# Kernel optimization log

Hardware: AMD Instinct MI355X
Metric: run time of the kernel (lower is better)

Reference implementation:

```python
import jax, jax.numpy as jnp
import numpy as np

R, N, B, S = 20, 4096, 16, 256          # relations, total nodes, graphs, nodes per graph
DIN, HID, H = 512, 128, 4               # in_dim, hidden_dim, num_heads
D = HID * H                              # flattened node-feature width (=512)
E = 16384                                # edges per relation
NEG_SLOPE = 0.2


def _gat(h, src, dst, W, al, ar, b):
    # DGL GATConv, eval mode (dropout off), identity residual (in == H*out), allow_zero_in_degree
    z = (h @ W).reshape(N, H, HID)                        # [N,H,Dh]
    el = (z * al).sum(-1)                                 # [N,H]
    er = (z * ar).sum(-1)                                 # [N,H]
    e = jax.nn.leaky_relu(el[src] + er[dst], NEG_SLOPE)   # [E,H]
    m = jax.ops.segment_max(e, dst, num_segments=N)       # per-dst max (edge softmax)
    ex = jnp.exp(e - m[dst])
    den = jax.ops.segment_sum(ex, dst, num_segments=N)
    alpha = ex / den[dst]                                 # [E,H]
    agg = jax.ops.segment_sum(alpha[..., None] * z[src], dst, num_segments=N)
    return agg + h.reshape(N, H, HID) + b, alpha


def _rgat_conv(h, src, dst, W, al, ar, b):
    # HeteroGraphConv with aggregate='mean' over R relations; scan keeps memory flat
    def body(acc, xs):
        s, d, Wr, alr, arr, br = xs
        out, alpha = _gat(h, s, d, Wr, alr, arr, br)
        return acc + out, alpha.mean(-1)                  # attention meaned over heads -> [E]
    acc, attn = jax.lax.scan(body, jnp.zeros((N, H, HID), h.dtype), (src, dst, W, al, ar, b))
    return acc / R, attn                                  # [N,H,Dh], [R,E]


def setup_inputs() -> dict:
    key = jax.random.key(0)
    ks = jax.random.split(key, 24)
    f32 = jnp.float32
    p = lambda k, shape: jax.random.normal(k, shape, f32) * 0.05
    z = lambda shape: jnp.zeros(shape, f32)
    return {
        'feat': jax.random.normal(ks[0], (N, DIN), f32),
        'hyp_emb': jax.random.normal(ks[1], (B, D), f32),
        'edge_src': jax.random.randint(ks[2], (R, E), 0, N),
        'edge_dst': jax.random.randint(ks[3], (R, E), 0, N),
        'W1': p(ks[4], (R, DIN, H * HID)), 'al1': p(ks[5], (R, H, HID)), 'ar1': p(ks[6], (R, H, HID)), 'b1': z((R, H, HID)),
        'W2': p(ks[7], (R, D, H * HID)), 'al2': p(ks[8], (R, H, HID)), 'ar2': p(ks[9], (R, H, HID)), 'b2': z((R, H, HID)),
        'Wq': p(ks[10], (D, D)), 'bq': z(D), 'Wk': p(ks[11], (D, D)), 'bk': z(D),
        'Wv': p(ks[12], (D, D)), 'bv': z(D), 'Wo': p(ks[13], (D, D)), 'bo': z(D),
        'Wn1': p(ks[14], (2 * D, HID)), 'bn1': z(HID), 'Wn2': p(ks[15], (HID, 2)), 'bn2': z(2),
    }


def reference(feat, hyp_emb, edge_src, edge_dst,
              W1, al1, ar1, b1, W2, al2, ar2, b2,
              Wq, bq, Wk, bk, Wv, bv, Wo, bo, Wn1, bn1, Wn2, bn2):
    # --- RGAT (rgat_generation) layer 1 + attention weights ---
    h1, attn = _rgat_conv(feat, edge_src, edge_dst, W1, al1, ar1, b1)
    h1 = jax.nn.elu(h1.reshape(N, D))
    # --- layer 2 ---
    h2, _ = _rgat_conv(h1, edge_src, edge_dst, W2, al2, ar2, b2)
    feats = h2.reshape(N, D)
    # --- node importance: scatter-add edge attention onto dst nodes, summed over etypes ---
    imp = jax.ops.segment_sum(attn.reshape(-1), edge_dst.reshape(-1), num_segments=N)
    feats_p = feats.reshape(B, S, D)                      # uniform graphs: split+pad == reshape
    weighted = feats_p * imp.reshape(B, S)[..., None]
    # --- MultiheadAttention(embed=D, heads=4): query = hyp_emb broadcast to all S positions ---
    Hm, Dm = 4, D // 4
    q = (hyp_emb @ Wq + bq).reshape(B, Hm, 1, Dm)         # identical query at every position
    k = (feats_p @ Wk + bk).reshape(B, S, Hm, Dm).transpose(0, 2, 1, 3)
    v = (feats_p @ Wv + bv).reshape(B, S, Hm, Dm).transpose(0, 2, 1, 3)
    scores = jnp.einsum('bhqd,bhkd->bhqk', q, k) / jnp.sqrt(jnp.float32(Dm))
    a = jax.nn.softmax(scores, axis=-1)                   # [B,Hm,1,S]
    ctx = jnp.einsum('bhqk,bhkd->bhqd', a, v).reshape(B, 1, D)
    attn_out = jnp.broadcast_to(ctx @ Wo + bo, (B, S, D))
    # --- node classifier on concat(weighted feats, attention output) ---
    combined = jnp.concatenate([weighted, attn_out], axis=-1).reshape(N, 2 * D)
    node_logits = jax.nn.relu(combined @ Wn1 + bn1) @ Wn2 + bn2
    return node_logits, attn
```

## Files before the change

kernel.cpp:

```cpp
#include <hip/hip_runtime.h>
#include <hip/hip_bf16.h>
#include <math.h>

#define NREL 20
#define NN   4096
#define NE   16384
#define DF   512
#define NHD  4
#define DHH  128
#define NB   16
#define NS   256

typedef __attribute__((ext_vector_type(8))) __bf16 bf16x8;
typedef __attribute__((ext_vector_type(4))) float f32x4;

__device__ inline float bf2f(unsigned short u) {
    union { float f; unsigned int i; } c; c.i = ((unsigned int)u) << 16; return c.f;
}
__device__ inline unsigned short f2bu(float f) {
    union { __hip_bfloat16 b; unsigned short u; } c; c.b = __float2bfloat16(f); return c.u;
}
__device__ inline void storeOut(float* p, float v) { *p = v; }
__device__ inline void storeOut(__hip_bfloat16* p, float v) { *p = __float2bfloat16(v); }

__device__ inline void load_lds16(const __hip_bfloat16* g, __hip_bfloat16* l) {
    __builtin_amdgcn_global_load_lds(
        (const __attribute__((address_space(1))) unsigned int*)(const void*)g,
        (__attribute__((address_space(3))) unsigned int*)(void*)l, 16, 0, 0);
}

__global__ void count_kernel(const int* __restrict__ dst, int* __restrict__ cnt) {
    int idx = blockIdx.x * 256 + threadIdx.x;
    int r = idx / NE;
    atomicAdd(&cnt[r * NN + dst[idx]], 1);
}

__global__ void sumcnt_kernel(const int* __restrict__ cnt, int* __restrict__ cntAll) {
    int n = blockIdx.x * 256 + threadIdx.x;
    int s = 0;
    #pragma unroll
    for (int r = 0; r < NREL; ++r) s += cnt[r * NN + n];
    cntAll[n] = s;
}

__global__ void scan_kernel(const int* __restrict__ cnt, int* __restrict__ rowptr,
                            int* __restrict__ woff) {
    int r = blockIdx.x;
    int t = threadIdx.x;
    __shared__ int sums[1024];
    int v[4]; int local = 0;
    #pragma unroll
    for (int j = 0; j < 4; ++j) { v[j] = cnt[r * NN + t * 4 + j]; local += v[j]; }
    sums[t] = local;
    __syncthreads();
    for (int off = 1; off < 1024; off <<= 1) {
        int x = (t >= off) ? sums[t - off] : 0;
        __syncthreads();
        sums[t] += x;
        __syncthreads();
    }
    int run = (t == 0) ? 0 : sums[t - 1];
    #pragma unroll
    for (int j = 0; j < 4; ++j) {
        rowptr[r * (NN + 1) + t * 4 + j] = run;
        woff[r * NN + t * 4 + j] = run;
        run += v[j];
    }
    if (t == 1023) rowptr[r * (NN + 1) + NN] = run;
}

__global__ void fill_kernel(const int* __restrict__ dst, const int* __restrict__ src,
                            int* __restrict__ woff, int* __restrict__ srcCSR,
                            int* __restrict__ eidCSR) {
    int idx = blockIdx.x * 256 + threadIdx.x;
    int r = idx / NE; int e = idx % NE;
    int pos = atomicAdd(&woff[r * NN + dst[idx]], 1);
    srcCSR[r * NE + pos] = src[idx];
    eidCSR[r * NE + pos] = e;
}

__global__ void cast_kernel(const float* __restrict__ in, unsigned short* __restrict__ out) {
    int i = blockIdx.x * 256 + threadIdx.x;
    float4 v = ((const float4*)in)[i];
    ushort4 o;
    o.x = f2bu(v.x); o.y = f2bu(v.y); o.z = f2bu(v.z); o.w = f2bu(v.w);
    ((ushort4*)out)[i] = o;
}

__global__ void biassum_kernel(const float* __restrict__ bmat, float* __restrict__ bsum) {
    int f = blockIdx.x * 256 + threadIdx.x;
    float s = 0.f;
    #pragma unroll
    for (int r = 0; r < NREL; ++r) s += bmat[r * DF + f];
    bsum[f] = s;
}

__global__ __launch_bounds__(256) void transw_kernel(
    const float* __restrict__ W, __hip_bfloat16* __restrict__ Wt, int K, int N)
{
    int r = blockIdx.z;
    __shared__ float t[32][33];
    int k0 = blockIdx.x * 32, n0 = blockIdx.y * 32;
    int tx = threadIdx.x % 32, ty = threadIdx.x / 32;
    #pragma unroll
    for (int kk = ty; kk < 32; kk += 8)
        t[kk][tx] = W[((size_t)r * K + k0 + kk) * N + n0 + tx];
    __syncthreads();
    #pragma unroll
    for (int nn = ty; nn < 32; nn += 8)
        Wt[((size_t)r * N + n0 + nn) * K + k0 + tx] = __float2bfloat16(t[tx][nn]);
}

template <typename OutT, bool RELU>
__global__ __launch_bounds__(256) void mfma_gemm(
    const __hip_bfloat16* __restrict__ A,
    const __hip_bfloat16* __restrict__ BtAll,
    const float* __restrict__ bias,
    OutT* __restrict__ Call, int M, int N, int K)
{
    int r = blockIdx.z;
    const __hip_bfloat16* Bt = BtAll + (size_t)r * N * K;
    OutT* C = Call + (size_t)r * M * N;
    const int rowBase = blockIdx.y * 128;
    const int colBase = blockIdx.x * 128;
    __shared__ __hip_bfloat16 As[128 * 32];
    __shared__ __hip_bfloat16 Bs[128 * 32];
    const int tid = threadIdx.x;
    const int w = tid >> 6, l = tid & 63;
    const int wr = w >> 1, wc = w & 1;
    const int m15 = l & 15, q = l >> 4;
    const int sRow = w * 16 + (l >> 2);
    const int sK = (l & 3) * 8;
    const __hip_bfloat16* Ag0 = A + (size_t)(rowBase + sRow) * K + sK;
    const __hip_bfloat16* Ag1 = Ag0 + (size_t)64 * K;
    const __hip_bfloat16* Bg0 = Bt + (size_t)(colBase + sRow) * K + sK;
    const __hip_bfloat16* Bg1 = Bg0 + (size_t)64 * K;
    __hip_bfloat16* Asl0 = As + sRow * 32 + sK;
    __hip_bfloat16* Asl1 = Asl0 + 2048;
    __hip_bfloat16* Bsl0 = Bs + sRow * 32 + sK;
    __hip_bfloat16* Bsl1 = Bsl0 + 2048;

    f32x4 acc[4][4];
    #pragma unroll
    for (int i = 0; i < 4; ++i)
        #pragma unroll
        for (int j = 0; j < 4; ++j) acc[i][j] = (f32x4){0.f, 0.f, 0.f, 0.f};

    for (int k0 = 0; k0 < K; k0 += 32) {
        load_lds16(Ag0 + k0, Asl0);
        load_lds16(Ag1 + k0, Asl1);
        load_lds16(Bg0 + k0, Bsl0);
        load_lds16(Bg1 + k0, Bsl1);
        __syncthreads();
        bf16x8 a[4], b[4];
        #pragma unroll
        for (int i = 0; i < 4; ++i)
            a[i] = *(const bf16x8*)&As[(wr * 64 + i * 16 + m15) * 32 + q * 8];
        #pragma unroll
        for (int j = 0; j < 4; ++j)
            b[j] = *(const bf16x8*)&Bs[(wc * 64 + j * 16 + m15) * 32 + q * 8];
        #pragma unroll
        for (int i = 0; i < 4; ++i)
            #pragma unroll
            for (int j = 0; j < 4; ++j)
                acc[i][j] = __builtin_amdgcn_mfma_f32_16x16x32_bf16(a[i], b[j], acc[i][j], 0, 0, 0);
        __syncthreads();
    }

    #pragma unroll
    for (int i = 0; i < 4; ++i) {
        #pragma unroll
        for (int j = 0; j < 4; ++j) {
            int col = colBase + wc * 64 + j * 16 + m15;
            float bv = bias ? bias[col] : 0.f;
            #pragma unroll
            for (int reg = 0; reg < 4; ++reg) {
                int row = rowBase + wr * 64 + i * 16 + q * 4 + reg;
                float v = acc[i][j][reg] + bv;
                if (RELU) v = fmaxf(v, 0.f);
                storeOut(&C[(size_t)row * N + col], v);
            }
        }
    }
}

template <typename OutT>
__global__ __launch_bounds__(256) void gemm_kernel(
    const float* __restrict__ A, const float* __restrict__ Bm,
    const float* __restrict__ bias, OutT* __restrict__ C,
    int M, int K, int Nn)
{
    int r = blockIdx.z;
    const float* B = Bm + (size_t)r * K * Nn;
    OutT* Cr = C + (size_t)r * M * Nn;
    int rowBase = blockIdx.y * 64;
    int colBase = blockIdx.x * 64;
    __shared__ float As[64][17];
    __shared__ float Bs[16][64];
    int tid = threadIdx.x;
    int tx = tid % 16, ty = tid / 16;
    float acc[4][4] = {};
    int aRow = tid / 4, aK4 = (tid % 4) * 4;
    int bK = tid / 16, bN4 = (tid % 16) * 4;
    for (int k0 = 0; k0 < K; k0 += 16) {
        int gRow = rowBase + aRow;
        float4 av = make_float4(0.f, 0.f, 0.f, 0.f);
        if (gRow < M) av = *(const float4*)(A + (size_t)gRow * K + k0 + aK4);
        As[aRow][aK4 + 0] = av.x; As[aRow][aK4 + 1] = av.y;
        As[aRow][aK4 + 2] = av.z; As[aRow][aK4 + 3] = av.w;
        float4 bv = *(const float4*)(B + (size_t)(k0 + bK) * Nn + colBase + bN4);
        *(float4*)&Bs[bK][bN4] = bv;
        __syncthreads();
        #pragma unroll
        for (int k = 0; k < 16; ++k) {
            float a[4], b[4];
            #pragma unroll
            for (int i = 0; i < 4; ++i) a[i] = As[ty * 4 + i][k];
            #pragma unroll
            for (int j = 0; j < 4; ++j) b[j] = Bs[k][tx * 4 + j];
            #pragma unroll
            for (int i = 0; i < 4; ++i)
                #pragma unroll
                for (int j = 0; j < 4; ++j) acc[i][j] += a[i] * b[j];
        }
        __syncthreads();
    }
    #pragma unroll
    for (int i = 0; i < 4; ++i) {
        int gRow = rowBase + ty * 4 + i;
        if (gRow >= M) continue;
        #pragma unroll
        for (int j = 0; j < 4; ++j) {
            int gCol = colBase + tx * 4 + j;
            float v = acc[i][j];
            if (bias) v += bias[gCol];
            storeOut(&Cr[(size_t)gRow * Nn + gCol], v);
        }
    }
}

__global__ __launch_bounds__(256) void eler_kernel(
    const __hip_bfloat16* __restrict__ Z, const float* __restrict__ al,
    const float* __restrict__ ar, float* __restrict__ el, float* __restrict__ er)
{
    int gw = (blockIdx.x * 256 + threadIdx.x) / 64;
    int lane = threadIdx.x & 63;
    int h = lane >> 4;
    int r = gw / NN, n = gw % NN;
    const __hip_bfloat16* zp = Z + ((size_t)(r * NN + n)) * DF + lane * 8;
    float4 raw = *(const float4*)zp;
    const unsigned short* u = (const unsigned short*)&raw;
    float pel = 0.f, per_ = 0.f;
    #pragma unroll
    for (int j = 0; j < 8; ++j) {
        int f = lane * 8 + j;
        float z = bf2f(u[j]);
        pel  += z * al[r * DF + f];
        per_ += z * ar[r * DF + f];
    }
    #pragma unroll
    for (int off = 1; off < 16; off <<= 1) {
        pel  += __shfl_xor(pel, off);
        per_ += __shfl_xor(per_, off);
    }
    if ((lane & 15) == 0) {
        el[((size_t)r * NN + n) * NHD + h] = pel;
        er[((size_t)r * NN + n) * NHD + h] = per_;
    }
}

__global__ __launch_bounds__(256) void alpha_kernel(
    const float* __restrict__ el, const float* __restrict__ er,
    const int* __restrict__ rowptr, const int* __restrict__ rowptr2,
    const int* __restrict__ cnt, const int* __restrict__ srcCSR,
    const int* __restrict__ eidCSR,
    float* __restrict__ alphaPk, int* __restrict__ srcPk,
    float* __restrict__ attn, float* __restrict__ imp)
{
    int t = blockIdx.x * 256 + threadIdx.x;
    int r = t / NN, n = t % NN;
    int start = rowptr[r * (NN + 1) + n];
    int d = rowptr[r * (NN + 1) + n + 1] - start;
    if (d == 0) return;
    float4 er4 = *(const float4*)&er[((size_t)r * NN + n) * NHD];
    float4 den = make_float4(0.f, 0.f, 0.f, 0.f);
    for (int j = 0; j < d; ++j) {
        int s = srcCSR[r * NE + start + j];
        float4 el4 = *(const float4*)&el[((size_t)r * NN + s) * NHD];
        float v0 = el4.x + er4.x; v0 = v0 > 0.f ? v0 : 0.2f * v0;
        float v1 = el4.y + er4.y; v1 = v1 > 0.f ? v1 : 0.2f * v1;
        float v2 = el4.z + er4.z; v2 = v2 > 0.f ? v2 : 0.2f * v2;
        float v3 = el4.w + er4.w; v3 = v3 > 0.f ? v3 : 0.2f * v3;
        den.x += __expf(v0); den.y += __expf(v1);
        den.z += __expf(v2); den.w += __expf(v3);
    }
    float4 inv = make_float4(1.f / den.x, 1.f / den.y, 1.f / den.z, 1.f / den.w);
    int pbase = rowptr2[n];
    for (int rp = 0; rp < r; ++rp) pbase += cnt[rp * NN + n];
    float impLoc = 0.f;
    for (int j = 0; j < d; ++j) {
        int s = srcCSR[r * NE + start + j];
        float4 el4 = *(const float4*)&el[((size_t)r * NN + s) * NHD];
        float v0 = el4.x + er4.x; v0 = v0 > 0.f ? v0 : 0.2f * v0;
        float v1 = el4.y + er4.y; v1 = v1 > 0.f ? v1 : 0.2f * v1;
        float v2 = el4.z + er4.z; v2 = v2 > 0.f ? v2 : 0.2f * v2;
        float v3 = el4.w + er4.w; v3 = v3 > 0.f ? v3 : 0.2f * v3;
        float4 a4 = make_float4(__expf(v0) * inv.x, __expf(v1) * inv.y,
                                __expf(v2) * inv.z, __expf(v3) * inv.w);
        *(float4*)&alphaPk[(size_t)(pbase + j) * 4] = a4;
        srcPk[pbase + j] = r * NN + s;
        if (attn) {
            float a = 0.25f * (a4.x + a4.y + a4.z + a4.w);
            attn[r * NE + eidCSR[r * NE + start + j]] = a;
            impLoc += a;
        }
    }
    if (attn) atomicAdd(&imp[n], impLoc);
}

__global__ __launch_bounds__(256) void aggc_kernel(
    const __hip_bfloat16* __restrict__ Z,
    const int* __restrict__ rowptr2, const int* __restrict__ srcPk,
    const float* __restrict__ alphaPk, const float* __restrict__ bsum,
    const float* __restrict__ hin, float* __restrict__ hout,
    __hip_bfloat16* __restrict__ hout_bf, int applyElu)
{
    int n = blockIdx.x;
    int w = threadIdx.x >> 6, lane = threadIdx.x & 63;
    int h = lane >> 4;
    int base = rowptr2[n];
    int deg = rowptr2[n + 1] - base;
    float acc[8] = {};
    int i = w;
    int nzrow = 0; float nalpha = 0.f;
    if (i < deg) {
        nzrow = srcPk[base + i];
        nalpha = alphaPk[(size_t)(base + i) * 4 + h];
    }
    while (i < deg) {
        int zrow = nzrow; float alpha = nalpha;
        int i2 = i + 4;
        if (i2 < deg) {
            nzrow = srcPk[base + i2];
            nalpha = alphaPk[(size_t)(base + i2) * 4 + h];
        }
        float4 raw = *(const float4*)&Z[(size_t)zrow * DF + lane * 8];
        const unsigned short* u = (const unsigned short*)&raw;
        #pragma unroll
        for (int j = 0; j < 8; ++j) acc[j] += alpha * bf2f(u[j]);
        i = i2;
    }
    __shared__ float red[4][DF];
    #pragma unroll
    for (int j = 0; j < 8; ++j) red[w][lane * 8 + j] = acc[j];
    __syncthreads();
    const float invR = 1.0f / NREL;
    int f = threadIdx.x;
    #pragma unroll
    for (int rep = 0; rep < 2; ++rep, f += 256) {
        float v = red[0][f] + red[1][f] + red[2][f] + red[3][f];
        v = (v + bsum[f]) * invR + hin[(size_t)n * DF + f];
        if (applyElu) v = v > 0.f ? v : expm1f(v);
        hout[(size_t)n * DF + f] = v;
        hout_bf[(size_t)n * DF + f] = __float2bfloat16(v);
    }
}

__global__ __launch_bounds__(256) void mha_scores(
    const float* __restrict__ q, const float* __restrict__ k,
    float* __restrict__ scores)
{
    int b = blockIdx.x;
    int w = threadIdx.x >> 6, lane = threadIdx.x & 63;
    int s = blockIdx.y * 4 + w;
    const float4* qp = (const float4*)&q[(size_t)b * DF + lane * 8];
    const float4* kp = (const float4*)&k[((size_t)(b * NS + s)) * DF + lane * 8];
    float4 q0 = qp[0], q1 = qp[1];
    float4 k0 = kp[0], k1 = kp[1];
    float p = q0.x * k0.x + q0.y * k0.y + q0.z * k0.z + q0.w * k0.w
            + q1.x * k1.x + q1.y * k1.y + q1.z * k1.z + q1.w * k1.w;
    #pragma unroll
    for (int off = 1; off < 16; off <<= 1) p += __shfl_xor(p, off);
    if ((lane & 15) == 0) {
        int h = lane >> 4;
        scores[((size_t)(b * NHD + h)) * NS + s] = p * 0.08838834764831845f;
    }
}

__global__ __launch_bounds__(256) void mha_soft(float* __restrict__ scores) {
    int b = blockIdx.x;
    int h = threadIdx.x >> 6, lane = threadIdx.x & 63;
    float* sp = &scores[((size_t)(b * NHD + h)) * NS];
    float v[4];
    float mx = -INFINITY;
    #pragma unroll
    for (int i = 0; i < 4; ++i) { v[i] = sp[lane + 64 * i]; mx = fmaxf(mx, v[i]); }
    #pragma unroll
    for (int off = 32; off; off >>= 1) mx = fmaxf(mx, __shfl_xor(mx, off));
    float sum = 0.f;
    #pragma unroll
    for (int i = 0; i < 4; ++i) { v[i] = __expf(v[i] - mx); sum += v[i]; }
    #pragma unroll
    for (int off = 32; off; off >>= 1) sum += __shfl_xor(sum, off);
    float inv = 1.0f / sum;
    #pragma unroll
    for (int i = 0; i < 4; ++i) sp[lane + 64 * i] = v[i] * inv;
}

__global__ __launch_bounds__(256) void mha_ctx(
    const float* __restrict__ scores, const float* __restrict__ v,
    float* __restrict__ ctx)
{
    int b = blockIdx.x, h = blockIdx.y;
    int t = threadIdx.x;
    int d = t & 127, half = t >> 7;
    __shared__ float a_s[NS];
    a_s[t] = scores[((size_t)(b * NHD + h)) * NS + t];
    __syncthreads();
    float acc = 0.f;
    const float* vp = &v[((size_t)(b * NS + half * 128)) * DF + h * DHH + d];
    #pragma unroll 4
    for (int i = 0; i < 128; ++i)
        acc += a_s[half * 128 + i] * vp[(size_t)i * DF];
    __shared__ float red[256];
    red[t] = acc;
    __syncthreads();
    if (t < 128) ctx[(size_t)b * DF + h * DHH + t] = red[t] + red[t + 128];
}

__global__ __launch_bounds__(256) void combined_kernel(
    const float* __restrict__ feats, const float* __restrict__ imp,
    const float* __restrict__ abuf, __hip_bfloat16* __restrict__ comb)
{
    int n = blockIdx.x;
    int t = threadIdx.x;
    int b = n >> 8;
    float im = imp[n];
    #pragma unroll
    for (int rep = 0; rep < 4; ++rep) {
        int f = t + rep * 256;
        float v = (f < DF) ? feats[(size_t)n * DF + f] * im
                           : abuf[(size_t)b * DF + (f - DF)];
        comb[(size_t)n * (2 * DF) + f] = __float2bfloat16(v);
    }
}

__global__ __launch_bounds__(256) void cls2_kernel(
    const float* __restrict__ hidden, const float* __restrict__ Wn2,
    const float* __restrict__ bn2, float* __restrict__ out)
{
    __shared__ float w2[256];
    int t = threadIdx.x;
    w2[t] = Wn2[t];
    __syncthreads();
    int n = blockIdx.x * 256 + t;
    const float* hp = &hidden[(size_t)n * 128];
    float p0 = bn2[0], p1 = bn2[1];
    #pragma unroll 4
    for (int kk = 0; kk < 128; ++kk) {
        float hv = hp[kk];
        p0 += hv * w2[kk * 2 + 0];
        p1 += hv * w2[kk * 2 + 1];
    }
    out[n * 2 + 0] = p0;
    out[n * 2 + 1] = p1;
}

extern "C" void kernel_launch(void* const* d_in, const int* in_sizes, int n_in,
                              void* d_out, int out_size, void* d_ws, size_t ws_size,
                              hipStream_t stream) {
    const float* feat = (const float*)d_in[0];
    const float* hyp  = (const float*)d_in[1];
    const int*   esrc = (const int*)d_in[2];
    const int*   edst = (const int*)d_in[3];
    const float* W1   = (const float*)d_in[4];
    const float* al1  = (const float*)d_in[5];
    const float* ar1  = (const float*)d_in[6];
    const float* b1   = (const float*)d_in[7];
    const float* W2   = (const float*)d_in[8];
    const float* al2  = (const float*)d_in[9];
    const float* ar2  = (const float*)d_in[10];
    const float* b2   = (const float*)d_in[11];
    const float* Wq = (const float*)d_in[12]; const float* bq = (const float*)d_in[13];
    const float* Wk = (const float*)d_in[14]; const float* bk = (const float*)d_in[15];
    const float* Wv = (const float*)d_in[16]; const float* bv = (const float*)d_in[17];
    const float* Wo = (const float*)d_in[18]; const float* bo = (const float*)d_in[19];
    const float* Wn1 = (const float*)d_in[20]; const float* bn1 = (const float*)d_in[21];
    const float* Wn2 = (const float*)d_in[22]; const float* bn2 = (const float*)d_in[23];

    char* ws = (char*)d_ws;
    size_t off = 0;
    auto alloc = [&](size_t bytes) -> void* {
        void* p = ws + off;
        off += (bytes + 255) & ~(size_t)255;
        return p;
    };
    __hip_bfloat16* Z = (__hip_bfloat16*)alloc((size_t)NREL * NN * DF * 2);
    float* el     = (float*)alloc((size_t)NREL * NN * NHD * 4);
    float* er     = (float*)alloc((size_t)NREL * NN * NHD * 4);
    int* rowptr   = (int*)alloc((size_t)NREL * (NN + 1) * 4);
    int* rowptr2  = (int*)alloc((size_t)(NN + 1) * 4);
    int* woff     = (int*)alloc((size_t)NREL * NN * 4);
    int* woff2    = (int*)alloc((size_t)NN * 4);
    int* srcCSR   = (int*)alloc((size_t)NREL * NE * 4);
    int* eidCSR   = (int*)alloc((size_t)NREL * NE * 4);
    int* cnt      = (int*)alloc((size_t)NREL * NN * 4);
    int* cntAll   = (int*)alloc((size_t)NN * 4);
    int* srcPk    = (int*)alloc((size_t)NREL * NE * 4);
    float* alphaPk= (float*)alloc((size_t)NREL * NE * NHD * 4);
    float* bsum   = (float*)alloc((size_t)DF * 4);
    float* h1     = (float*)alloc((size_t)NN * DF * 4);
    float* feats  = (float*)alloc((size_t)NN * DF * 4);
    float* imp    = (float*)alloc((size_t)NN * 4);
    float* kbuf   = (float*)alloc((size_t)NN * DF * 4);
    float* vbuf   = (float*)alloc((size_t)NN * DF * 4);
    float* qbuf   = (float*)alloc((size_t)NB * DF * 4);
    float* ctxb   = (float*)alloc((size_t)NB * DF * 4);
    float* abuf   = (float*)alloc((size_t)NB * DF * 4);
    float* scoresb= (float*)alloc((size_t)NB * NHD * NS * 4);
    float* hidden = (float*)alloc((size_t)NN * 128 * 4);
    __hip_bfloat16* featbf  = (__hip_bfloat16*)alloc((size_t)NN * DF * 2);
    __hip_bfloat16* h1bf    = (__hip_bfloat16*)alloc((size_t)NN * DF * 2);
    __hip_bfloat16* featsbf = (__hip_bfloat16*)alloc((size_t)NN * DF * 2);
    __hip_bfloat16* combbf  = (__hip_bfloat16*)alloc((size_t)NN * 2 * DF * 2);
    __hip_bfloat16* Wt1 = (__hip_bfloat16*)alloc((size_t)NREL * DF * DF * 2);
    __hip_bfloat16* Wt2 = (__hip_bfloat16*)alloc((size_t)NREL * DF * DF * 2);
    __hip_bfloat16* WtK = (__hip_bfloat16*)alloc((size_t)DF * DF * 2);
    __hip_bfloat16* WtV = (__hip_bfloat16*)alloc((size_t)DF * DF * 2);
    __hip_bfloat16* Wn1t = (__hip_bfloat16*)alloc((size_t)(2 * DF) * 128 * 2);
    if (off > ws_size) return;

    float* logits = (float*)d_out;
    float* attn   = (float*)d_out + (size_t)NN * 2;

    hipMemsetAsync(cnt, 0, (size_t)NREL * NN * 4, stream);
    hipMemsetAsync(imp, 0, (size_t)NN * 4, stream);
    count_kernel<<<NREL * NE / 256, 256, 0, stream>>>(edst, cnt);
    sumcnt_kernel<<<NN / 256, 256, 0, stream>>>(cnt, cntAll);
    scan_kernel<<<NREL, 1024, 0, stream>>>(cnt, rowptr, woff);
    scan_kernel<<<1, 1024, 0, stream>>>(cntAll, rowptr2, woff2);
    fill_kernel<<<NREL * NE / 256, 256, 0, stream>>>(edst, esrc, woff, srcCSR, eidCSR);

    cast_kernel<<<NN * DF / 1024, 256, 0, stream>>>(feat, (unsigned short*)featbf);
    transw_kernel<<<dim3(DF / 32, DF / 32, NREL), 256, 0, stream>>>(W1, Wt1, DF, DF);
    transw_kernel<<<dim3(DF / 32, DF / 32, NREL), 256, 0, stream>>>(W2, Wt2, DF, DF);
    transw_kernel<<<dim3(DF / 32, DF / 32, 1), 256, 0, stream>>>(Wk, WtK, DF, DF);
    transw_kernel<<<dim3(DF / 32, DF / 32, 1), 256, 0, stream>>>(Wv, WtV, DF, DF);
    transw_kernel<<<dim3(2 * DF / 32, 128 / 32, 1), 256, 0, stream>>>(Wn1, Wn1t, 2 * DF, 128);

    mfma_gemm<__hip_bfloat16, false><<<dim3(DF / 128, NN / 128, NREL), 256, 0, stream>>>(
        featbf, Wt1, nullptr, Z, NN, DF, DF);
    eler_kernel<<<NREL * NN / 4, 256, 0, stream>>>(Z, al1, ar1, el, er);
    biassum_kernel<<<DF / 256, 256, 0, stream>>>(b1, bsum);
    alpha_kernel<<<NREL * NN / 256, 256, 0, stream>>>(
        el, er, rowptr, rowptr2, cnt, srcCSR, eidCSR, alphaPk, srcPk, attn, imp);
    aggc_kernel<<<NN, 256, 0, stream>>>(Z, rowptr2, srcPk, alphaPk, bsum,
                                        feat, h1, h1bf, 1);

    mfma_gemm<__hip_bfloat16, false><<<dim3(DF / 128, NN / 128, NREL), 256, 0, stream>>>(
        h1bf, Wt2, nullptr, Z, NN, DF, DF);
    eler_kernel<<<NREL * NN / 4, 256, 0, stream>>>(Z, al2, ar2, el, er);
    biassum_kernel<<<DF / 256, 256, 0, stream>>>(b2, bsum);
    alpha_kernel<<<NREL * NN / 256, 256, 0, stream>>>(
        el, er, rowptr, rowptr2, cnt, srcCSR, eidCSR, alphaPk, srcPk, nullptr, nullptr);
    aggc_kernel<<<NN, 256, 0, stream>>>(Z, rowptr2, srcPk, alphaPk, bsum,
                                        h1, feats, featsbf, 0);

    mfma_gemm<float, false><<<dim3(DF / 128, NN / 128, 1), 256, 0, stream>>>(
        featsbf, WtK, bk, kbuf, NN, DF, DF);
    mfma_gemm<float, false><<<dim3(DF / 128, NN / 128, 1), 256, 0, stream>>>(
        featsbf, WtV, bv, vbuf, NN, DF, DF);
    gemm_kernel<float><<<dim3(DF / 64, 1, 1), 256, 0, stream>>>(
        hyp, Wq, bq, qbuf, NB, DF, DF);
    mha_scores<<<dim3(NB, NS / 4), 256, 0, stream>>>(qbuf, kbuf, scoresb);
    mha_soft<<<NB, 256, 0, stream>>>(scoresb);
    mha_ctx<<<dim3(NB, NHD), 256, 0, stream>>>(scoresb, vbuf, ctxb);
    gemm_kernel<float><<<dim3(DF / 64, 1, 1), 256, 0, stream>>>(
        ctxb, Wo, bo, abuf, NB, DF, DF);

    combined_kernel<<<NN, 256, 0, stream>>>(feats, imp, abuf, combbf);
    mfma_gemm<float, true><<<dim3(1, NN / 128, 1), 256, 0, stream>>>(
        combbf, Wn1t, bn1, hidden, NN, 128, 2 * DF);
    cls2_kernel<<<NN / 256, 256, 0, stream>>>(hidden, Wn2, bn2, logits);
}
```

Baseline: 682.3 us.

## Fuse el/er attention projections into GEMM epilogue, swizzle LDS, unroll aggregation

The per-relation GEMM epilogue now computes the el/er dot products directly from the fp32 accumulators, reducing them with lane shuffles and shared memory. This removes the separate eler kernel, which re-read the whole bf16 Z tensor. The GEMM also gets an XOR swizzle on the LDS k-chunk offsets to cut bank conflicts on fragment reads. The aggregation loop now processes two neighbour rows per iteration to raise memory-level parallelism. As a side effect, el/er come from unrounded fp32 values rather than bf16 Z, and the epilogue adds extra register pressure and a sync.

```diff
diff --git a/kernel.cpp b/kernel.cpp
--- a/kernel.cpp
+++ b/kernel.cpp
@@ -111,12 +111,14 @@
         Wt[((size_t)r * N + n0 + nn) * K + k0 + tx] = __float2bfloat16(t[tx][nn]);
 }
 
-template <typename OutT, bool RELU>
+template <typename OutT, bool RELU, bool FUSE>
 __global__ __launch_bounds__(256) void mfma_gemm(
     const __hip_bfloat16* __restrict__ A,
     const __hip_bfloat16* __restrict__ BtAll,
     const float* __restrict__ bias,
-    OutT* __restrict__ Call, int M, int N, int K)
+    OutT* __restrict__ Call, int M, int N, int K,
+    const float* __restrict__ al, const float* __restrict__ ar,
+    float* __restrict__ el, float* __restrict__ er)
 {
     int r = blockIdx.z;
     const __hip_bfloat16* Bt = BtAll + (size_t)r * N * K;
@@ -130,15 +132,16 @@
     const int wr = w >> 1, wc = w & 1;
     const int m15 = l & 15, q = l >> 4;
     const int sRow = w * 16 + (l >> 2);
-    const int sK = (l & 3) * 8;
-    const __hip_bfloat16* Ag0 = A + (size_t)(rowBase + sRow) * K + sK;
+    const int sKs = (((l & 3) ^ ((l >> 3) & 3))) * 8;
+    const __hip_bfloat16* Ag0 = A + (size_t)(rowBase + sRow) * K + sKs;
     const __hip_bfloat16* Ag1 = Ag0 + (size_t)64 * K;
-    const __hip_bfloat16* Bg0 = Bt + (size_t)(colBase + sRow) * K + sK;
+    const __hip_bfloat16* Bg0 = Bt + (size_t)(colBase + sRow) * K + sKs;
     const __hip_bfloat16* Bg1 = Bg0 + (size_t)64 * K;
-    __hip_bfloat16* Asl0 = As + sRow * 32 + sK;
+    __hip_bfloat16* Asl0 = As + sRow * 32 + (l & 3) * 8;
     __hip_bfloat16* Asl1 = Asl0 + 2048;
-    __hip_bfloat16* Bsl0 = Bs + sRow * 32 + sK;
+    __hip_bfloat16* Bsl0 = Bs + sRow * 32 + (l & 3) * 8;
     __hip_bfloat16* Bsl1 = Bsl0 + 2048;
+    const int swf = (m15 >> 1) & 3;
 
     f32x4 acc[4][4];
     #pragma unroll
@@ -155,10 +158,10 @@
         bf16x8 a[4], b[4];
         #pragma unroll
         for (int i = 0; i < 4; ++i)
-            a[i] = *(const bf16x8*)&As[(wr * 64 + i * 16 + m15) * 32 + q * 8];
+            a[i] = *(const bf16x8*)&As[(wr * 64 + i * 16 + m15) * 32 + (q ^ swf) * 8];
         #pragma unroll
         for (int j = 0; j < 4; ++j)
-            b[j] = *(const bf16x8*)&Bs[(wc * 64 + j * 16 + m15) * 32 + q * 8];
+            b[j] = *(const bf16x8*)&Bs[(wc * 64 + j * 16 + m15) * 32 + (q ^ swf) * 8];
         #pragma unroll
         for (int i = 0; i < 4; ++i)
             #pragma unroll
@@ -180,6 +183,57 @@
                 if (RELU) v = fmaxf(v, 0.f);
                 storeOut(&C[(size_t)row * N + col], v);
             }
+        }
+    }
+
+    if (FUSE) {
+        float alv[4], arv[4];
+        #pragma unroll
+        for (int j = 0; j < 4; ++j) {
+            int col = colBase + wc * 64 + j * 16 + m15;
+            alv[j] = al[r * DF + col];
+            arv[j] = ar[r * DF + col];
+        }
+        float pe[4][4], pr[4][4];
+        #pragma unroll
+        for (int i = 0; i < 4; ++i)
+            #pragma unroll
+            for (int reg = 0; reg < 4; ++reg) {
+                float se = 0.f, sr = 0.f;
+                #pragma unroll
+                for (int j = 0; j < 4; ++j) {
+                    se += acc[i][j][reg] * alv[j];
+                    sr += acc[i][j][reg] * arv[j];
+                }
+                pe[i][reg] = se; pr[i][reg] = sr;
+            }
+        #pragma unroll
+        for (int off = 1; off < 16; off <<= 1)
+            #pragma unroll
+            for (int i = 0; i < 4; ++i)
+                #pragma unroll
+                for (int reg = 0; reg < 4; ++reg) {
+                    pe[i][reg] += __shfl_xor(pe[i][reg], off);
+                    pr[i][reg] += __shfl_xor(pr[i][reg], off);
+                }
+        float* eP = (float*)As;
+        float* rP = eP + 256;
+        if (m15 == 0) {
+            #pragma unroll
+            for (int i = 0; i < 4; ++i)
+                #pragma unroll
+                for (int reg = 0; reg < 4; ++reg) {
+                    int rowL = wr * 64 + i * 16 + q * 4 + reg;
+                    eP[rowL * 2 + wc] = pe[i][reg];
+                    rP[rowL * 2 + wc] = pr[i][reg];
+                }
+        }
+        __syncthreads();
+        if (tid < 128) {
+            int head = colBase >> 7;
+            size_t idx = ((size_t)r * NN + rowBase + tid) * NHD + head;
+            el[idx] = eP[tid * 2] + eP[tid * 2 + 1];
+            er[idx] = rP[tid * 2] + rP[tid * 2 + 1];
         }
     }
 }
@@ -239,36 +293,6 @@
     }
 }
 
-__global__ __launch_bounds__(256) void eler_kernel(
-    const __hip_bfloat16* __restrict__ Z, const float* __restrict__ al,
-    const float* __restrict__ ar, float* __restrict__ el, float* __restrict__ er)
-{
-    int gw = (blockIdx.x * 256 + threadIdx.x) / 64;
-    int lane = threadIdx.x & 63;
-    int h = lane >> 4;
-    int r = gw / NN, n = gw % NN;
-    const __hip_bfloat16* zp = Z + ((size_t)(r * NN + n)) * DF + lane * 8;
-    float4 raw = *(const float4*)zp;
-    const unsigned short* u = (const unsigned short*)&raw;
-    float pel = 0.f, per_ = 0.f;
-    #pragma unroll
-    for (int j = 0; j < 8; ++j) {
-        int f = lane * 8 + j;
-        float z = bf2f(u[j]);
-        pel  += z * al[r * DF + f];
-        per_ += z * ar[r * DF + f];
-    }
-    #pragma unroll
-    for (int off = 1; off < 16; off <<= 1) {
-        pel  += __shfl_xor(pel, off);
-        per_ += __shfl_xor(per_, off);
-    }
-    if ((lane & 15) == 0) {
-        el[((size_t)r * NN + n) * NHD + h] = pel;
-        er[((size_t)r * NN + n) * NHD + h] = per_;
-    }
-}
-
 __global__ __launch_bounds__(256) void alpha_kernel(
     const float* __restrict__ el, const float* __restrict__ er,
     const int* __restrict__ rowptr, const int* __restrict__ rowptr2,
@@ -331,24 +355,23 @@
     int base = rowptr2[n];
     int deg = rowptr2[n + 1] - base;
     float acc[8] = {};
-    int i = w;
-    int nzrow = 0; float nalpha = 0.f;
-    if (i < deg) {
-        nzrow = srcPk[base + i];
-        nalpha = alphaPk[(size_t)(base + i) * 4 + h];
-    }
+    int i = w * 2;
+    int z0 = 0, z1 = 0; float a0 = 0.f, a1 = 0.f;
+    if (i < deg)     { z0 = srcPk[base + i];     a0 = alphaPk[(size_t)(base + i) * 4 + h]; }
+    if (i + 1 < deg) { z1 = srcPk[base + i + 1]; a1 = alphaPk[(size_t)(base + i + 1) * 4 + h]; }
     while (i < deg) {
-        int zrow = nzrow; float alpha = nalpha;
-        int i2 = i + 4;
-        if (i2 < deg) {
-            nzrow = srcPk[base + i2];
-            nalpha = alphaPk[(size_t)(base + i2) * 4 + h];
-        }
-        float4 raw = *(const float4*)&Z[(size_t)zrow * DF + lane * 8];
-        const unsigned short* u = (const unsigned short*)&raw;
-        #pragma unroll
-        for (int j = 0; j < 8; ++j) acc[j] += alpha * bf2f(u[j]);
-        i = i2;
+        int cz0 = z0, cz1 = z1; float ca0 = a0, ca1 = a1;
+        int ni = i + 8;
+        if (ni < deg)     { z0 = srcPk[base + ni];     a0 = alphaPk[(size_t)(base + ni) * 4 + h]; }
+        if (ni + 1 < deg) { z1 = srcPk[base + ni + 1]; a1 = alphaPk[(size_t)(base + ni + 1) * 4 + h]; }
+        else a1 = 0.f;
+        float4 r0 = *(const float4*)&Z[(size_t)cz0 * DF + lane * 8];
+        float4 r1 = *(const float4*)&Z[(size_t)cz1 * DF + lane * 8];
+        const unsigned short* u0 = (const unsigned short*)&r0;
+        const unsigned short* u1 = (const unsigned short*)&r1;
+        #pragma unroll
+        for (int j = 0; j < 8; ++j) acc[j] += ca0 * bf2f(u0[j]) + ca1 * bf2f(u1[j]);
+        i = ni;
     }
     __shared__ float red[4][DF];
     #pragma unroll
@@ -548,28 +571,26 @@
     transw_kernel<<<dim3(DF / 32, DF / 32, 1), 256, 0, stream>>>(Wv, WtV, DF, DF);
     transw_kernel<<<dim3(2 * DF / 32, 128 / 32, 1), 256, 0, stream>>>(Wn1, Wn1t, 2 * DF, 128);
 
-    mfma_gemm<__hip_bfloat16, false><<<dim3(DF / 128, NN / 128, NREL), 256, 0, stream>>>(
-        featbf, Wt1, nullptr, Z, NN, DF, DF);
-    eler_kernel<<<NREL * NN / 4, 256, 0, stream>>>(Z, al1, ar1, el, er);
+    mfma_gemm<__hip_bfloat16, false, true><<<dim3(DF / 128, NN / 128, NREL), 256, 0, stream>>>(
+        featbf, Wt1, nullptr, Z, NN, DF, DF, al1, ar1, el, er);
     biassum_kernel<<<DF / 256, 256, 0, stream>>>(b1, bsum);
     alpha_kernel<<<NREL * NN / 256, 256, 0, stream>>>(
         el, er, rowptr, rowptr2, cnt, srcCSR, eidCSR, alphaPk, srcPk, attn, imp);
     aggc_kernel<<<NN, 256, 0, stream>>>(Z, rowptr2, srcPk, alphaPk, bsum,
                                         feat, h1, h1bf, 1);
 
-    mfma_gemm<__hip_bfloat16, false><<<dim3(DF / 128, NN / 128, NREL), 256, 0, stream>>>(
-        h1bf, Wt2, nullptr, Z, NN, DF, DF);
-    eler_kernel<<<NREL * NN / 4, 256, 0, stream>>>(Z, al2, ar2, el, er);
+    mfma_gemm<__hip_bfloat16, false, true><<<dim3(DF / 128, NN / 128, NREL), 256, 0, stream>>>(
+        h1bf, Wt2, nullptr, Z, NN, DF, DF, al2, ar2, el, er);
     biassum_kernel<<<DF / 256, 256, 0, stream>>>(b2, bsum);
     alpha_kernel<<<NREL * NN / 256, 256, 0, stream>>>(
         el, er, rowptr, rowptr2, cnt, srcCSR, eidCSR, alphaPk, srcPk, nullptr, nullptr);
     aggc_kernel<<<NN, 256, 0, stream>>>(Z, rowptr2, srcPk, alphaPk, bsum,
                                         h1, feats, featsbf, 0);
 
-    mfma_gemm<float, false><<<dim3(DF / 128, NN / 128, 1), 256, 0, stream>>>(
-        featsbf, WtK, bk, kbuf, NN, DF, DF);
-    mfma_gemm<float, false><<<dim3(DF / 128, NN / 128, 1), 256, 0, stream>>>(
-        featsbf, WtV, bv, vbuf, NN, DF, DF);
+    mfma_gemm<float, false, false><<<dim3(DF / 128, NN / 128, 1), 256, 0, stream>>>(
+        featsbf, WtK, bk, kbuf, NN, DF, DF, nullptr, nullptr, nullptr, nullptr);
+    mfma_gemm<float, false, false><<<dim3(DF / 128, NN / 128, 1), 256, 0, stream>>>(
+        featsbf, WtV, bv, vbuf, NN, DF, DF, nullptr, nullptr, nullptr, nullptr);
     gemm_kernel<float><<<dim3(DF / 64, 1, 1), 256, 0, stream>>>(
         hyp, Wq, bq, qbuf, NB, DF, DF);
     mha_scores<<<dim3(NB, NS / 4), 256, 0, stream>>>(qbuf, kbuf, scoresb);
@@ -579,7 +600,7 @@
         ctxb, Wo, bo, abuf, NB, DF, DF);
 
     combined_kernel<<<NN, 256, 0, stream>>>(feats, imp, abuf, combbf);
-    mfma_gemm<float, true><<<dim3(1, NN / 128, 1), 256, 0, stream>>>(
-        combbf, Wn1t, bn1, hidden, NN, 128, 2 * DF);
+    mfma_gemm<float, true, false><<<dim3(1, NN / 128, 1), 256, 0, stream>>>(
+        combbf, Wn1t, bn1, hidden, NN, 128, 2 * DF, nullptr, nullptr, nullptr, nullptr);
     cls2_kernel<<<NN / 256, 256, 0, stream>>>(hidden, Wn2, bn2, logits);
 }
```

After: 666.1 us. 1.02x faster.
